# Kernel tuning notes

Measured on AMD Instinct MI355X. Metric: run time of the kernel, lower is better.

Reference implementation:

```python
import jax, jax.numpy as jnp
import numpy as np

SIGMA = 1.0
TOP_K = 4

def setup_inputs() -> dict:
    key = jax.random.key(0)
    k1, k2, k3, k4 = jax.random.split(key, 4)
    B, N, IN_DIM, OUT_DIM, P = 2, 4096, 128, 128, 3
    x = jax.random.normal(k1, (B, N, IN_DIM), dtype=jnp.float32)
    pos = jax.random.normal(k2, (B, N, P), dtype=jnp.float32)
    # Linear(in_dim, out_dim): W [in_dim, out_dim], b [out_dim]
    lim = 1.0 / np.sqrt(IN_DIM)
    W = jax.random.uniform(k3, (IN_DIM, OUT_DIM), minval=-lim, maxval=lim, dtype=jnp.float32)
    b = jax.random.uniform(k4, (OUT_DIM,), minval=-lim, maxval=lim, dtype=jnp.float32)
    return {"x": x, "pos": pos, "W": W, "b": b}

def reference(x, pos, W, b):
    B, N, _ = x.shape
    # pairwise distances [B, N, N]
    pos_diff = pos[:, :, None, :] - pos[:, None, :, :]
    dist = jnp.sqrt(jnp.sum(pos_diff ** 2, axis=-1) + 1e-8)
    adj = jnp.exp(-dist ** 2 / (2.0 * SIGMA ** 2))
    # top-k mask along last dim
    _, indices = jax.lax.top_k(adj, TOP_K)  # [B, N, k]
    b_idx = jnp.arange(B)[:, None, None]
    n_idx = jnp.arange(N)[None, :, None]
    mask = jnp.zeros_like(adj).at[b_idx, n_idx, indices].set(1.0)
    adj = adj * mask
    adj = adj / (jnp.sum(adj, axis=-1, keepdims=True) + 1e-8)
    # weighted aggregation + linear
    out = jnp.einsum('bnm,bmd->bnd', adj, x)
    return out @ W + b
```

## Files before the change

### kernel.cpp

```cpp
#include <hip/hip_runtime.h>
#include <hip/hip_bf16.h>

#define NPTS 4096
#define NROWS 8192
#define DIM 128
#define GEMM_BLOCKS 1024

typedef __attribute__((ext_vector_type(8))) short bf16x8;
typedef __attribute__((ext_vector_type(4))) float f32x4;

__global__ __launch_bounds__(256) void k1_prep_gemm(const float* __restrict__ x,
                                                    const float* __restrict__ pos,
                                                    const float* __restrict__ W,
                                                    float4* __restrict__ pos4,
                                                    __hip_bfloat16* __restrict__ xWb) {
    int b = blockIdx.x;
    if (b >= GEMM_BLOCKS) {
        int t = (b - GEMM_BLOCKS) * 256 + threadIdx.x;
        const float* p = pos + (size_t)t * 3;
        pos4[t] = make_float4(p[0], p[1], p[2], 0.f);
        return;
    }
    int wave = threadIdx.x >> 6;
    int lane = threadIdx.x & 63;
    int tile = b * 4 + wave;
    int m0 = (tile >> 3) << 4;
    int n0 = (tile & 7) << 4;
    int r = lane & 15;
    int kg = lane >> 4;
    const float* xr = x + (size_t)(m0 + r) * DIM + kg * 8;
    const float* wc = W + (size_t)(kg * 8) * DIM + (n0 + r);
    f32x4 acc = {0.f, 0.f, 0.f, 0.f};
    union { __hip_bfloat16 h; short s; } u;
#pragma unroll
    for (int kb = 0; kb < 4; ++kb) {
        float4 a0 = *(const float4*)(xr + kb * 32);
        float4 a1 = *(const float4*)(xr + kb * 32 + 4);
        bf16x8 af, bf;
        u.h = __float2bfloat16(a0.x); af[0] = u.s;
        u.h = __float2bfloat16(a0.y); af[1] = u.s;
        u.h = __float2bfloat16(a0.z); af[2] = u.s;
        u.h = __float2bfloat16(a0.w); af[3] = u.s;
        u.h = __float2bfloat16(a1.x); af[4] = u.s;
        u.h = __float2bfloat16(a1.y); af[5] = u.s;
        u.h = __float2bfloat16(a1.z); af[6] = u.s;
        u.h = __float2bfloat16(a1.w); af[7] = u.s;
#pragma unroll
        for (int i = 0; i < 8; ++i) {
            u.h = __float2bfloat16(wc[(size_t)(kb * 32 + i) * DIM]);
            bf[i] = u.s;
        }
        acc = __builtin_amdgcn_mfma_f32_16x16x32_bf16(af, bf, acc, 0, 0, 0);
    }
    int col = n0 + r;
    int rbase = m0 + (kg << 2);
#pragma unroll
    for (int reg = 0; reg < 4; ++reg)
        xWb[(size_t)(rbase + reg) * DIM + col] = __float2bfloat16(acc[reg]);
}

__device__ __forceinline__ double mkkey(float d2, int j) {
    return __longlong_as_double(__double_as_longlong((double)d2) |
                                (unsigned long long)(unsigned)j);
}

__device__ __forceinline__ void kins(double& k0, double& k1, double& k2,
                                     double& k3, double s) {
    double c = fmax(k0, s); k0 = fmin(k0, s);
    double t = fmax(k1, c); k1 = fmin(k1, c); c = t;
    t = fmax(k2, c);        k2 = fmin(k2, c); c = t;
    k3 = fmin(k3, c);
}

__device__ __forceinline__ void kmerge(double& a0, double& a1, double& a2,
                                       double& a3, double b0, double b1,
                                       double b2, double b3) {
    double m0 = fmin(a0, b3), m1 = fmin(a1, b2);
    double m2 = fmin(a2, b1), m3 = fmin(a3, b0);
    double t0 = fmin(m0, m2), t2 = fmax(m0, m2);
    double t1 = fmin(m1, m3), t3 = fmax(m1, m3);
    a0 = fmin(t0, t1); a1 = fmax(t0, t1);
    a2 = fmin(t2, t3); a3 = fmax(t2, t3);
}

__global__ __launch_bounds__(256) void topk_agg(const float4* __restrict__ pos4,
                                                const __hip_bfloat16* __restrict__ xWb,
                                                const float* __restrict__ bias,
                                                float* __restrict__ out) {
    int lane = threadIdx.x & 63;
    int wave = threadIdx.x >> 6;
    int group = wave >> 1;
    int half = wave & 1;
    int rowbase = blockIdx.x * 4 + group * 2;
    int batch = rowbase >> 12;
    int ibase = rowbase & (NPTS - 1);
    const float4* pb = pos4 + (size_t)batch * NPTS;

    float4 q0 = pb[ibase], q1 = pb[ibase + 1];
    const double INF = __builtin_inf();
    double a0 = INF, a1 = INF, a2 = INF, a3 = INF;
    double b0 = INF, b1 = INF, b2 = INF, b3 = INF;

    int jbase = (half << 11) + lane;
#pragma unroll 8
    for (int t = 0; t < 32; ++t) {
        int j = jbase + (t << 6);
        float4 p = pb[j];
        float dx = q0.x - p.x, dy = q0.y - p.y, dz = q0.z - p.z;
        float d2 = fmaf(dx, dx, fmaf(dy, dy, dz * dz));
        kins(a0, a1, a2, a3, mkkey(d2, j));
        dx = q1.x - p.x; dy = q1.y - p.y; dz = q1.z - p.z;
        d2 = fmaf(dx, dx, fmaf(dy, dy, dz * dz));
        kins(b0, b1, b2, b3, mkkey(d2, j));
    }

#pragma unroll
    for (int off = 1; off < 64; off <<= 1) {
        double p0 = __shfl_xor(a0, off), p1 = __shfl_xor(a1, off);
        double p2 = __shfl_xor(a2, off), p3 = __shfl_xor(a3, off);
        kmerge(a0, a1, a2, a3, p0, p1, p2, p3);
        p0 = __shfl_xor(b0, off); p1 = __shfl_xor(b1, off);
        p2 = __shfl_xor(b2, off); p3 = __shfl_xor(b3, off);
        kmerge(b0, b1, b2, b3, p0, p1, p2, p3);
    }

    __shared__ double lds[2][2][2][4];
    if (lane == 0) {
        lds[group][half][0][0] = a0; lds[group][half][0][1] = a1;
        lds[group][half][0][2] = a2; lds[group][half][0][3] = a3;
        lds[group][half][1][0] = b0; lds[group][half][1][1] = b1;
        lds[group][half][1][2] = b2; lds[group][half][1][3] = b3;
    }
    __syncthreads();
    if (half) return;

    kmerge(a0, a1, a2, a3, lds[group][1][0][0], lds[group][1][0][1],
                           lds[group][1][0][2], lds[group][1][0][3]);
    kmerge(b0, b1, b2, b3, lds[group][1][1][0], lds[group][1][1][1],
                           lds[group][1][1][2], lds[group][1][1][3]);

    int c = lane << 1;
    float2 bb = *(const float2*)(bias + c);
    const unsigned short* xu = (const unsigned short*)xWb;
    size_t bbase = ((size_t)batch * NPTS) << 7;
#pragma unroll
    for (int k = 0; k < 2; ++k) {
        double k0 = k ? b0 : a0, k1 = k ? b1 : a1;
        double k2 = k ? b2 : a2, k3 = k ? b3 : a3;
        unsigned i0 = (unsigned)__double_as_longlong(k0) & 0xFFFu;
        unsigned i1 = (unsigned)__double_as_longlong(k1) & 0xFFFu;
        unsigned i2 = (unsigned)__double_as_longlong(k2) & 0xFFFu;
        unsigned i3 = (unsigned)__double_as_longlong(k3) & 0xFFFu;
        float d0 = (float)k0, d1 = (float)k1, d2 = (float)k2, d3 = (float)k3;
        float w0 = __expf(-(d0 + 1e-8f) * 0.5f);
        float w1 = __expf(-(d1 + 1e-8f) * 0.5f);
        float w2 = __expf(-(d2 + 1e-8f) * 0.5f);
        float w3 = __expf(-(d3 + 1e-8f) * 0.5f);
        float inv = 1.0f / (w0 + w1 + w2 + w3 + 1e-8f);
        w0 *= inv; w1 *= inv; w2 *= inv; w3 *= inv;
        ushort2 g0 = *(const ushort2*)(xu + bbase + ((size_t)i0 << 7) + c);
        ushort2 g1 = *(const ushort2*)(xu + bbase + ((size_t)i1 << 7) + c);
        ushort2 g2 = *(const ushort2*)(xu + bbase + ((size_t)i2 << 7) + c);
        ushort2 g3 = *(const ushort2*)(xu + bbase + ((size_t)i3 << 7) + c);
        float ox = bb.x + w0 * __uint_as_float((unsigned)g0.x << 16)
                        + w1 * __uint_as_float((unsigned)g1.x << 16)
                        + w2 * __uint_as_float((unsigned)g2.x << 16)
                        + w3 * __uint_as_float((unsigned)g3.x << 16);
        float oy = bb.y + w0 * __uint_as_float((unsigned)g0.y << 16)
                        + w1 * __uint_as_float((unsigned)g1.y << 16)
                        + w2 * __uint_as_float((unsigned)g2.y << 16)
                        + w3 * __uint_as_float((unsigned)g3.y << 16);
        *(float2*)(out + (((size_t)(rowbase + k)) << 7) + c) = make_float2(ox, oy);
    }
}

extern "C" void kernel_launch(void* const* d_in, const int* in_sizes, int n_in,
                              void* d_out, int out_size, void* d_ws, size_t ws_size,
                              hipStream_t stream) {
    const float* x    = (const float*)d_in[0];
    const float* pos  = (const float*)d_in[1];
    const float* W    = (const float*)d_in[2];
    const float* bias = (const float*)d_in[3];
    float* out = (float*)d_out;

    char* ws = (char*)d_ws;
    __hip_bfloat16* xWb = (__hip_bfloat16*)ws;
    float4* pos4 = (float4*)(ws + (size_t)NROWS * DIM * 2);

    k1_prep_gemm<<<GEMM_BLOCKS + NROWS / 256, 256, 0, stream>>>(x, pos, W, pos4, xWb);
    topk_agg<<<NROWS / 4, 256, 0, stream>>>(pos4, xWb, bias, out);
}
```

Measured before the change: 88.78 us.

## Stage positions in LDS tiles and give each wave full candidate scan

The top-k kernel now copies the raw xyz positions in 2048-point tiles into shared memory, and each wave scans all 4096 candidates for its two query rows. This replaces the per-lane global float4 loads and removes the cross-wave LDS merge. The pos-to-float4 packing pass is dropped from the first kernel, which now only does the GEMM. Each block handles 8 rows instead of 4, so there are half as many blocks. The cost is a serial scan twice as long per wave, plus two block barriers per tile and possible stride-3 LDS bank conflicts.

```diff
diff --git a/kernel.cpp b/kernel.cpp
--- a/kernel.cpp
+++ b/kernel.cpp
@@ -4,26 +4,18 @@
 #define NPTS 4096
 #define NROWS 8192
 #define DIM 128
+#define TILE 2048
 #define GEMM_BLOCKS 1024
 
 typedef __attribute__((ext_vector_type(8))) short bf16x8;
 typedef __attribute__((ext_vector_type(4))) float f32x4;
 
-__global__ __launch_bounds__(256) void k1_prep_gemm(const float* __restrict__ x,
-                                                    const float* __restrict__ pos,
-                                                    const float* __restrict__ W,
-                                                    float4* __restrict__ pos4,
-                                                    __hip_bfloat16* __restrict__ xWb) {
-    int b = blockIdx.x;
-    if (b >= GEMM_BLOCKS) {
-        int t = (b - GEMM_BLOCKS) * 256 + threadIdx.x;
-        const float* p = pos + (size_t)t * 3;
-        pos4[t] = make_float4(p[0], p[1], p[2], 0.f);
-        return;
-    }
+__global__ __launch_bounds__(256) void xw_mfma(const float* __restrict__ x,
+                                               const float* __restrict__ W,
+                                               __hip_bfloat16* __restrict__ xWb) {
     int wave = threadIdx.x >> 6;
     int lane = threadIdx.x & 63;
-    int tile = b * 4 + wave;
+    int tile = blockIdx.x * 4 + wave;
     int m0 = (tile >> 3) << 4;
     int n0 = (tile & 7) << 4;
     int r = lane & 15;
@@ -83,35 +75,50 @@
     a2 = fmin(t2, t3); a3 = fmax(t2, t3);
 }
 
-__global__ __launch_bounds__(256) void topk_agg(const float4* __restrict__ pos4,
+__global__ __launch_bounds__(256) void topk_agg(const float* __restrict__ pos,
                                                 const __hip_bfloat16* __restrict__ xWb,
                                                 const float* __restrict__ bias,
                                                 float* __restrict__ out) {
+    __shared__ float sp[TILE * 3];
     int lane = threadIdx.x & 63;
     int wave = threadIdx.x >> 6;
-    int group = wave >> 1;
-    int half = wave & 1;
-    int rowbase = blockIdx.x * 4 + group * 2;
+    int rowbase = blockIdx.x * 8;
     int batch = rowbase >> 12;
     int ibase = rowbase & (NPTS - 1);
-    const float4* pb = pos4 + (size_t)batch * NPTS;
+    const float* pb = pos + (size_t)batch * NPTS * 3;
 
-    float4 q0 = pb[ibase], q1 = pb[ibase + 1];
+    int r0 = ibase + wave * 2;
+    float q0x = pb[3 * r0 + 0], q0y = pb[3 * r0 + 1], q0z = pb[3 * r0 + 2];
+    float q1x = pb[3 * r0 + 3], q1y = pb[3 * r0 + 4], q1z = pb[3 * r0 + 5];
+
     const double INF = __builtin_inf();
     double a0 = INF, a1 = INF, a2 = INF, a3 = INF;
     double b0 = INF, b1 = INF, b2 = INF, b3 = INF;
 
-    int jbase = (half << 11) + lane;
-#pragma unroll 8
-    for (int t = 0; t < 32; ++t) {
-        int j = jbase + (t << 6);
-        float4 p = pb[j];
-        float dx = q0.x - p.x, dy = q0.y - p.y, dz = q0.z - p.z;
-        float d2 = fmaf(dx, dx, fmaf(dy, dy, dz * dz));
-        kins(a0, a1, a2, a3, mkkey(d2, j));
-        dx = q1.x - p.x; dy = q1.y - p.y; dz = q1.z - p.z;
-        d2 = fmaf(dx, dx, fmaf(dy, dy, dz * dz));
-        kins(b0, b1, b2, b3, mkkey(d2, j));
+    for (int tile = 0; tile < 2; ++tile) {
+        const float4* src = (const float4*)(pb + (size_t)tile * TILE * 3);
+        float4* dst = (float4*)sp;
+#pragma unroll
+        for (int i = 0; i < 6; ++i)
+            dst[threadIdx.x * 6 + i] = src[threadIdx.x * 6 + i];
+        __syncthreads();
+
+        int jb = tile * TILE + lane;
+#pragma unroll 4
+        for (int it = 0; it < TILE / 64; ++it) {
+            int jj = it * 64 + lane;
+            float px = sp[3 * jj + 0];
+            float py = sp[3 * jj + 1];
+            float pz = sp[3 * jj + 2];
+            int j = jb + it * 64;
+            float dx = q0x - px, dy = q0y - py, dz = q0z - pz;
+            float d2 = fmaf(dx, dx, fmaf(dy, dy, dz * dz));
+            kins(a0, a1, a2, a3, mkkey(d2, j));
+            dx = q1x - px; dy = q1y - py; dz = q1z - pz;
+            d2 = fmaf(dx, dx, fmaf(dy, dy, dz * dz));
+            kins(b0, b1, b2, b3, mkkey(d2, j));
+        }
+        __syncthreads();
     }
 
 #pragma unroll
@@ -123,21 +130,6 @@
         p2 = __shfl_xor(b2, off); p3 = __shfl_xor(b3, off);
         kmerge(b0, b1, b2, b3, p0, p1, p2, p3);
     }
-
-    __shared__ double lds[2][2][2][4];
-    if (lane == 0) {
-        lds[group][half][0][0] = a0; lds[group][half][0][1] = a1;
-        lds[group][half][0][2] = a2; lds[group][half][0][3] = a3;
-        lds[group][half][1][0] = b0; lds[group][half][1][1] = b1;
-        lds[group][half][1][2] = b2; lds[group][half][1][3] = b3;
-    }
-    __syncthreads();
-    if (half) return;
-
-    kmerge(a0, a1, a2, a3, lds[group][1][0][0], lds[group][1][0][1],
-                           lds[group][1][0][2], lds[group][1][0][3]);
-    kmerge(b0, b1, b2, b3, lds[group][1][1][0], lds[group][1][1][1],
-                           lds[group][1][1][2], lds[group][1][1][3]);
 
     int c = lane << 1;
     float2 bb = *(const float2*)(bias + c);
@@ -170,7 +162,8 @@
                         + w1 * __uint_as_float((unsigned)g1.y << 16)
                         + w2 * __uint_as_float((unsigned)g2.y << 16)
                         + w3 * __uint_as_float((unsigned)g3.y << 16);
-        *(float2*)(out + (((size_t)(rowbase + k)) << 7) + c) = make_float2(ox, oy);
+        *(float2*)(out + (((size_t)(rowbase + wave * 2 + k)) << 7) + c) =
+            make_float2(ox, oy);
     }
 }
 
@@ -183,10 +176,8 @@
     const float* bias = (const float*)d_in[3];
     float* out = (float*)d_out;
 
-    char* ws = (char*)d_ws;
-    __hip_bfloat16* xWb = (__hip_bfloat16*)ws;
-    float4* pos4 = (float4*)(ws + (size_t)NROWS * DIM * 2);
+    __hip_bfloat16* xWb = (__hip_bfloat16*)d_ws;
 
-    k1_prep_gemm<<<GEMM_BLOCKS + NROWS / 256, 256, 0, stream>>>(x, pos, W, pos4, xWb);
-    topk_agg<<<NROWS / 4, 256, 0, stream>>>(pos4, xWb, bias, out);
+    xw_mfma<<<GEMM_BLOCKS, 256, 0, stream>>>(x, W, xWb);
+    topk_agg<<<NROWS / 8, 256, 0, stream>>>(pos, xWb, bias, out);
 }
```

New measurement: 88.04 us. Within noise of the previous version (-0.8%).
